# Optimization experiments

Measured on AMD Instinct MI355X. Metric: run time of the kernel, lower is better.

Reference implementation:

```python
import jax, jax.numpy as jnp
import numpy as np

THRESH = 0.1
BN_EPS = 1e-5
B, N, C_IN, C_HID, C_OUT = 4096, 128, 64, 256, 128


def setup_inputs() -> dict:
    key = jax.random.key(0)
    ks = jax.random.split(key, 10)
    a = jax.random.uniform(ks[0], (B, N, N), dtype=jnp.float32)
    v = jax.random.normal(ks[1], (B, N, C_IN), dtype=jnp.float32)
    # MLP params: Linear(C_IN->C_HID) + BN + ReLU + Linear(C_HID->C_OUT) + BN + ReLU
    W1 = jax.random.normal(ks[2], (C_IN, C_HID), dtype=jnp.float32) / np.sqrt(C_IN)
    b1 = jnp.zeros((C_HID,), jnp.float32)
    g1 = 1.0 + 0.1 * jax.random.normal(ks[3], (C_HID,), dtype=jnp.float32)
    be1 = 0.1 * jax.random.normal(ks[4], (C_HID,), dtype=jnp.float32)
    rm1 = 0.1 * jax.random.normal(ks[5], (C_HID,), dtype=jnp.float32)
    rv1 = jnp.ones((C_HID,), jnp.float32)
    W2 = jax.random.normal(ks[6], (C_HID, C_OUT), dtype=jnp.float32) / np.sqrt(C_HID)
    b2 = jnp.zeros((C_OUT,), jnp.float32)
    g2 = 1.0 + 0.1 * jax.random.normal(ks[7], (C_OUT,), dtype=jnp.float32)
    be2 = 0.1 * jax.random.normal(ks[8], (C_OUT,), dtype=jnp.float32)
    rm2 = 0.1 * jax.random.normal(ks[9], (C_OUT,), dtype=jnp.float32)
    rv2 = jnp.ones((C_OUT,), jnp.float32)
    return {"a": a, "v": v, "W1": W1, "b1": b1, "g1": g1, "be1": be1, "rm1": rm1, "rv1": rv1,
            "W2": W2, "b2": b2, "g2": g2, "be2": be2, "rm2": rm2, "rv2": rv2}


def reference(a, v, W1, b1, g1, be1, rm1, rv1, W2, b2, g2, be2, rm2, rv2):
    # threshold adjacency
    a_th = (a >= THRESH).astype(v.dtype)            # [B, N, N]
    # D^-0.5 A D^-0.5 as row/col rescaling (equivalent to diag_embed + bmm)
    d_inv_sqrt = jnp.sum(a_th, axis=-1) ** -0.5     # [B, N]
    a_bar = d_inv_sqrt[:, :, None] * a_th * d_inv_sqrt[:, None, :]
    # propagate
    h = jnp.einsum('bnm,bmc->bnc', a_bar, v)        # [B, N, C_IN]
    x = h.reshape(-1, h.shape[-1])                  # [(B N), C_IN]
    # MLP with BatchNorm in eval mode (running stats), dropout is identity in eval
    x = x @ W1 + b1
    x = (x - rm1) * jax.lax.rsqrt(rv1 + BN_EPS) * g1 + be1
    x = jax.nn.relu(x)
    x = x @ W2 + b2
    x = (x - rm2) * jax.lax.rsqrt(rv2 + BN_EPS) * g2 + be2
    x = jax.nn.relu(x)
    return x
```

## Files before the change

### kernel.cpp

```cpp
#include <hip/hip_runtime.h>


#define THRESH 0.1f
#define BN_EPS 1e-5f

typedef __attribute__((ext_vector_type(8))) short bf16x8;
typedef __attribute__((ext_vector_type(4))) float f32x4;

__device__ __forceinline__ unsigned short f2bf(float f) {
    union { float f; unsigned u; } x; x.f = f;
    unsigned r = x.u + 0x7FFFu + ((x.u >> 16) & 1u);
    return (unsigned short)(r >> 16);
}

__device__ __forceinline__ unsigned cvt_pk(float lo, float hi) {
    unsigned r;
    asm("v_cvt_pk_bf16_f32 %0, %1, %2" : "=v"(r) : "v"(lo), "v"(hi));
    return r;
}

__global__ void gcn_prep(const float* __restrict__ W1, const float* __restrict__ b1,
                         const float* __restrict__ g1, const float* __restrict__ be1,
                         const float* __restrict__ rm1, const float* __restrict__ rv1,
                         const float* __restrict__ W2, const float* __restrict__ b2,
                         const float* __restrict__ g2, const float* __restrict__ be2,
                         const float* __restrict__ rm2, const float* __restrict__ rv2,
                         unsigned short* __restrict__ W1s, unsigned short* __restrict__ W2s,
                         float* __restrict__ sh1, float* __restrict__ sh2) {
    int t = blockIdx.x * blockDim.x + threadIdx.x;
    if (t < 256 * 64) {
        int n = t >> 6, kp = t & 63;
        int sp = kp >> 3, lo = kp & 7;
        int s  = sp ^ (n & 7);
        int k2 = s * 8 + lo;
        int r = k2 & 3, aa = (k2 >> 2) & 1, gg = (k2 >> 3) & 3, T = k2 >> 5;
        int k = T * 32 + aa * 16 + gg * 4 + r;
        float sc = g1[n] * rsqrtf(rv1[n] + BN_EPS);
        W1s[t] = f2bf(W1[k * 256 + n] * sc);
    }
    {
        int n = t >> 8, kp = t & 255;
        int sp = kp >> 3, lo = kp & 7;
        int s  = sp ^ (n & 7);
        int k2 = s * 8 + lo;
        int r = k2 & 3, aa = (k2 >> 2) & 1, gg = (k2 >> 3) & 3, T = k2 >> 5;
        int k = T * 32 + aa * 16 + gg * 4 + r;
        float sc = g2[n] * rsqrtf(rv2[n] + BN_EPS);
        W2s[t] = f2bf(W2[k * 128 + n] * sc);
    }
    if (t < 256) {
        float s = g1[t] * rsqrtf(rv1[t] + BN_EPS);
        sh1[t] = (b1[t] - rm1[t]) * s + be1[t];
    }
    if (t < 128) {
        float s = g2[t] * rsqrtf(rv2[t] + BN_EPS);
        sh2[t] = (b2[t] - rm2[t]) * s + be2[t];
    }
}

__global__ void __launch_bounds__(256, 5)
gcn_prop(const float* __restrict__ A, const float* __restrict__ V,
         unsigned short* __restrict__ hP) {
    __shared__ unsigned short s_vtt[64 * 136];

    const int t    = threadIdx.x;
    const int lane = t & 63;
    const int w    = t >> 6;
    const int r16  = lane & 15;
    const int g    = lane >> 4;
    const int b    = blockIdx.x;

    const int mloc  = lane & 31;
    const int chalf = (lane >> 5) * 32;
    const float* vb = V + (size_t)b * 8192 + (size_t)(32 * w + mloc) * 64 + chalf;
    f32x4 pv[8];
#pragma unroll
    for (int q = 0; q < 8; ++q) pv[q] = *(const f32x4*)(vb + 4 * q);

    const float* ab = A + (size_t)b * 16384 + (size_t)(32 * w + r16) * 128;
    bf16x8 afrag[2][4];
    int cnt0 = 0, cnt1 = 0;
#pragma unroll
    for (int mt = 0; mt < 2; ++mt)
#pragma unroll
        for (int ks = 0; ks < 4; ++ks) {
            const float* p = ab + mt * 2048 + ks * 32 + 8 * g;
            f32x4 x0 = *(const f32x4*)p;
            f32x4 x1 = *(const f32x4*)(p + 4);
            union { unsigned short s[8]; bf16x8 v; } u;
            u.s[0] = (x0.x >= THRESH) ? (unsigned short)0x3F80u : (unsigned short)0u;
            u.s[1] = (x0.y >= THRESH) ? (unsigned short)0x3F80u : (unsigned short)0u;
            u.s[2] = (x0.z >= THRESH) ? (unsigned short)0x3F80u : (unsigned short)0u;
            u.s[3] = (x0.w >= THRESH) ? (unsigned short)0x3F80u : (unsigned short)0u;
            u.s[4] = (x1.x >= THRESH) ? (unsigned short)0x3F80u : (unsigned short)0u;
            u.s[5] = (x1.y >= THRESH) ? (unsigned short)0x3F80u : (unsigned short)0u;
            u.s[6] = (x1.z >= THRESH) ? (unsigned short)0x3F80u : (unsigned short)0u;
            u.s[7] = (x1.w >= THRESH) ? (unsigned short)0x3F80u : (unsigned short)0u;
            afrag[mt][ks] = u.v;
            int c = (x0.x >= THRESH) + (x0.y >= THRESH) + (x0.z >= THRESH) + (x0.w >= THRESH)
                  + (x1.x >= THRESH) + (x1.y >= THRESH) + (x1.z >= THRESH) + (x1.w >= THRESH);
            if (mt == 0) cnt0 += c; else cnt1 += c;
        }
    cnt0 += __shfl_xor(cnt0, 16); cnt0 += __shfl_xor(cnt0, 32);
    cnt1 += __shfl_xor(cnt1, 16); cnt1 += __shfl_xor(cnt1, 32);
    const float dinv0 = rsqrtf((float)cnt0);
    const float dinv1 = rsqrtf((float)cnt1);

    {
        float dm = (lane & 16) ? dinv1 : dinv0;
        int m = 32 * w + mloc;
#pragma unroll
        for (int q = 0; q < 8; ++q) {
            int c = chalf + 4 * q;
            s_vtt[(c + 0) * 136 + m] = f2bf(pv[q].x * dm);
            s_vtt[(c + 1) * 136 + m] = f2bf(pv[q].y * dm);
            s_vtt[(c + 2) * 136 + m] = f2bf(pv[q].z * dm);
            s_vtt[(c + 3) * 136 + m] = f2bf(pv[q].w * dm);
        }
    }
    __syncthreads();

    f32x4 acc1[4][2];
#pragma unroll
    for (int ct = 0; ct < 4; ++ct)
#pragma unroll
        for (int mt = 0; mt < 2; ++mt) acc1[ct][mt] = f32x4{0.f, 0.f, 0.f, 0.f};
#pragma unroll
    for (int ks = 0; ks < 4; ++ks)
#pragma unroll
        for (int ct = 0; ct < 4; ++ct) {
            bf16x8 av = *(const bf16x8*)(s_vtt + (ct * 16 + r16) * 136 + ks * 32 + 8 * g);
            acc1[ct][0] = __builtin_amdgcn_mfma_f32_16x16x32_bf16(av, afrag[0][ks], acc1[ct][0], 0, 0, 0);
            acc1[ct][1] = __builtin_amdgcn_mfma_f32_16x16x32_bf16(av, afrag[1][ks], acc1[ct][1], 0, 0, 0);
        }

#pragma unroll
    for (int mt = 0; mt < 2; ++mt) {
        float d = (mt == 0) ? dinv0 : dinv1;
        size_t m = (size_t)(b * 128 + 32 * w + 16 * mt + r16);
#pragma unroll
        for (int ks2 = 0; ks2 < 2; ++ks2) {
            union { unsigned u[4]; bf16x8 v; } pk;
            pk.u[0] = cvt_pk(acc1[2 * ks2][mt][0] * d,     acc1[2 * ks2][mt][1] * d);
            pk.u[1] = cvt_pk(acc1[2 * ks2][mt][2] * d,     acc1[2 * ks2][mt][3] * d);
            pk.u[2] = cvt_pk(acc1[2 * ks2 + 1][mt][0] * d, acc1[2 * ks2 + 1][mt][1] * d);
            pk.u[3] = cvt_pk(acc1[2 * ks2 + 1][mt][2] * d, acc1[2 * ks2 + 1][mt][3] * d);
            *(bf16x8*)(hP + m * 64 + ks2 * 32 + 8 * g) = pk.v;
        }
    }
}

__global__ void __launch_bounds__(512, 2)
gcn_mlp(const unsigned short* __restrict__ hP,
        const unsigned short* __restrict__ W1s, const unsigned short* __restrict__ W2s,
        const float* __restrict__ sh1g, const float* __restrict__ sh2g,
        float* __restrict__ out) {
    __shared__ char smem[99840];
    unsigned short* W1L = (unsigned short*)smem;
    unsigned short* W2L = (unsigned short*)(smem + 32768);
    float* s_sh1 = (float*)(smem + 98304);
    float* s_sh2 = (float*)(smem + 99328);

    const int t    = threadIdx.x;
    const int lane = t & 63;
    const int w    = t >> 6;
    const int r16  = lane & 15;
    const int g    = lane >> 4;

#pragma unroll
    for (int q = 0; q < 4; ++q)
        *(f32x4*)(smem + t * 64 + q * 16) = *(const f32x4*)((const char*)W1s + t * 64 + q * 16);
#pragma unroll
    for (int q = 0; q < 8; ++q)
        *(f32x4*)(smem + 32768 + t * 128 + q * 16) =
            *(const f32x4*)((const char*)W2s + t * 128 + q * 16);
    if (t < 256) s_sh1[t] = sh1g[t];
    if (t < 128) s_sh2[t] = sh2g[t];
    __syncthreads();

    const size_t row00 = (size_t)blockIdx.x * 1024;

    bf16x8 nb[2][2];
    {
        size_t mb = row00 + 32 * w;
#pragma unroll
        for (int mt = 0; mt < 2; ++mt)
#pragma unroll
            for (int ks2 = 0; ks2 < 2; ++ks2)
                nb[mt][ks2] = *(const bf16x8*)(hP + (mb + 16 * mt + r16) * 64 + ks2 * 32 + 8 * g);
    }

#pragma unroll 1
    for (int i = 0; i < 4; ++i) {
        bf16x8 bh[2][2];
#pragma unroll
        for (int mt = 0; mt < 2; ++mt)
#pragma unroll
            for (int ks2 = 0; ks2 < 2; ++ks2) bh[mt][ks2] = nb[mt][ks2];

        if (i < 3) {
            size_t mb = row00 + (i + 1) * 256 + 32 * w;
#pragma unroll
            for (int mt = 0; mt < 2; ++mt)
#pragma unroll
                for (int ks2 = 0; ks2 < 2; ++ks2)
                    nb[mt][ks2] = *(const bf16x8*)(hP + (mb + 16 * mt + r16) * 64 + ks2 * 32 + 8 * g);
        }

        f32x4 acc3[2][8];
#pragma unroll
        for (int mt = 0; mt < 2; ++mt)
#pragma unroll
            for (int ct = 0; ct < 8; ++ct) acc3[mt][ct] = f32x4{0.f, 0.f, 0.f, 0.f};

#pragma unroll
        for (int T = 0; T < 8; ++T) {
            f32x4 a2[2][2];
#pragma unroll
            for (int mt = 0; mt < 2; ++mt)
#pragma unroll
                for (int ctp = 0; ctp < 2; ++ctp) a2[mt][ctp] = f32x4{0.f, 0.f, 0.f, 0.f};
#pragma unroll
            for (int ctp = 0; ctp < 2; ++ctp) {
                int n = (2 * T + ctp) * 16 + r16;
#pragma unroll
                for (int ks2 = 0; ks2 < 2; ++ks2) {
                    int sp = (ks2 * 4 + g) ^ (n & 7);
                    bf16x8 aw = *(const bf16x8*)(W1L + n * 64 + sp * 8);
                    a2[0][ctp] = __builtin_amdgcn_mfma_f32_16x16x32_bf16(aw, bh[0][ks2], a2[0][ctp], 0, 0, 0);
                    a2[1][ctp] = __builtin_amdgcn_mfma_f32_16x16x32_bf16(aw, bh[1][ks2], a2[1][ctp], 0, 0, 0);
                }
            }
            unsigned wds[2][4];
#pragma unroll
            for (int ctp = 0; ctp < 2; ++ctp) {
                f32x4 sh = *(const f32x4*)(s_sh1 + (2 * T + ctp) * 16 + 4 * g);
#pragma unroll
                for (int mt = 0; mt < 2; ++mt) {
                    float y0 = fmaxf(a2[mt][ctp][0] + sh.x, 0.f);
                    float y1 = fmaxf(a2[mt][ctp][1] + sh.y, 0.f);
                    float y2 = fmaxf(a2[mt][ctp][2] + sh.z, 0.f);
                    float y3 = fmaxf(a2[mt][ctp][3] + sh.w, 0.f);
                    wds[mt][2 * ctp + 0] = cvt_pk(y0, y1);
                    wds[mt][2 * ctp + 1] = cvt_pk(y2, y3);
                }
            }
#pragma unroll
            for (int ct3 = 0; ct3 < 8; ++ct3) {
                int n  = ct3 * 16 + r16;
                int sp = (T * 4 + g) ^ (n & 7);
                bf16x8 bw = *(const bf16x8*)(W2L + n * 256 + sp * 8);
#pragma unroll
                for (int mt = 0; mt < 2; ++mt) {
                    union { unsigned u[4]; bf16x8 v; } af;
                    af.u[0] = wds[mt][0]; af.u[1] = wds[mt][1];
                    af.u[2] = wds[mt][2]; af.u[3] = wds[mt][3];
                    acc3[mt][ct3] = __builtin_amdgcn_mfma_f32_16x16x32_bf16(af.v, bw, acc3[mt][ct3], 0, 0, 0);
                }
            }
        }

        float* ob = out + (row00 + i * 256 + 32 * w) * 128;
#pragma unroll
        for (int ct3 = 0; ct3 < 8; ++ct3) {
            int c = ct3 * 16 + r16;
            float sh = s_sh2[c];
#pragma unroll
            for (int mt = 0; mt < 2; ++mt)
#pragma unroll
                for (int r = 0; r < 4; ++r) {
                    int row = 16 * mt + 4 * g + r;
                    ob[row * 128 + c] = fmaxf(acc3[mt][ct3][r] + sh, 0.f);
                }
        }
    }
}

extern "C" void kernel_launch(void* const* d_in, const int* in_sizes, int n_in,
                              void* d_out, int out_size, void* d_ws, size_t ws_size,
                              hipStream_t stream) {
    (void)in_sizes; (void)n_in; (void)out_size; (void)ws_size;
    const float* a   = (const float*)d_in[0];
    const float* v   = (const float*)d_in[1];
    const float* W1  = (const float*)d_in[2];
    const float* b1  = (const float*)d_in[3];
    const float* g1  = (const float*)d_in[4];
    const float* be1 = (const float*)d_in[5];
    const float* rm1 = (const float*)d_in[6];
    const float* rv1 = (const float*)d_in[7];
    const float* W2  = (const float*)d_in[8];
    const float* b2  = (const float*)d_in[9];
    const float* g2  = (const float*)d_in[10];
    const float* be2 = (const float*)d_in[11];
    const float* rm2 = (const float*)d_in[12];
    const float* rv2 = (const float*)d_in[13];

    char* ws = (char*)d_ws;
    unsigned short* W1s = (unsigned short*)ws;
    unsigned short* W2s = (unsigned short*)(ws + 32768);
    float* sh1 = (float*)(ws + 98304);
    float* sh2 = (float*)(ws + 99328);
    unsigned short* hP = (unsigned short*)(ws + 102400);

    gcn_prep<<<128, 256, 0, stream>>>(W1, b1, g1, be1, rm1, rv1,
                                      W2, b2, g2, be2, rm2, rv2,
                                      W1s, W2s, sh1, sh2);
    gcn_prop<<<4096, 256, 0, stream>>>(a, v, hP);
    gcn_mlp<<<512, 512, 0, stream>>>(hP, W1s, W2s, sh1, sh2, (float*)d_out);
}
```

Before: 227.0 us.

## Double per-wave row tile in MLP kernel and drop hP prefetch

Each wave in the MLP kernel now handles 64 rows (four 16-row M tiles) instead of 32, so every W1/W2 fragment read from LDS feeds twice as many MFMAs. The grid is halved to 256 blocks, each covering 2048 rows. The software prefetch of the next hP tile is removed and inputs are loaded at the start of each iteration. This trades higher register pressure (the acc3 accumulators double to 128 floats per lane), fewer blocks per CU for latency hiding, and exposed load latency for lower LDS traffic per MFMA.

Result: slower. 428.3 us (+88.7%).

```diff
diff --git a/kernel.cpp b/kernel.cpp
--- a/kernel.cpp
+++ b/kernel.cpp
@@ -178,46 +178,30 @@
     if (t < 128) s_sh2[t] = sh2g[t];
     __syncthreads();
 
-    const size_t row00 = (size_t)blockIdx.x * 1024;
-
-    bf16x8 nb[2][2];
-    {
-        size_t mb = row00 + 32 * w;
-#pragma unroll
-        for (int mt = 0; mt < 2; ++mt)
-#pragma unroll
-            for (int ks2 = 0; ks2 < 2; ++ks2)
-                nb[mt][ks2] = *(const bf16x8*)(hP + (mb + 16 * mt + r16) * 64 + ks2 * 32 + 8 * g);
-    }
+    const size_t row00 = (size_t)blockIdx.x * 2048;
 
 #pragma unroll 1
     for (int i = 0; i < 4; ++i) {
-        bf16x8 bh[2][2];
-#pragma unroll
-        for (int mt = 0; mt < 2; ++mt)
-#pragma unroll
-            for (int ks2 = 0; ks2 < 2; ++ks2) bh[mt][ks2] = nb[mt][ks2];
-
-        if (i < 3) {
-            size_t mb = row00 + (i + 1) * 256 + 32 * w;
-#pragma unroll
-            for (int mt = 0; mt < 2; ++mt)
-#pragma unroll
-                for (int ks2 = 0; ks2 < 2; ++ks2)
-                    nb[mt][ks2] = *(const bf16x8*)(hP + (mb + 16 * mt + r16) * 64 + ks2 * 32 + 8 * g);
-        }
-
-        f32x4 acc3[2][8];
-#pragma unroll
-        for (int mt = 0; mt < 2; ++mt)
+        const size_t mb = row00 + (size_t)i * 512 + 64 * w;
+
+        bf16x8 bh[4][2];
+#pragma unroll
+        for (int mt = 0; mt < 4; ++mt)
+#pragma unroll
+            for (int ks2 = 0; ks2 < 2; ++ks2)
+                bh[mt][ks2] = *(const bf16x8*)(hP + (mb + 16 * mt + r16) * 64 + ks2 * 32 + 8 * g);
+
+        f32x4 acc3[4][8];
+#pragma unroll
+        for (int mt = 0; mt < 4; ++mt)
 #pragma unroll
             for (int ct = 0; ct < 8; ++ct) acc3[mt][ct] = f32x4{0.f, 0.f, 0.f, 0.f};
 
 #pragma unroll
         for (int T = 0; T < 8; ++T) {
-            f32x4 a2[2][2];
-#pragma unroll
-            for (int mt = 0; mt < 2; ++mt)
+            f32x4 a2[4][2];
+#pragma unroll
+            for (int mt = 0; mt < 4; ++mt)
 #pragma unroll
                 for (int ctp = 0; ctp < 2; ++ctp) a2[mt][ctp] = f32x4{0.f, 0.f, 0.f, 0.f};
 #pragma unroll
@@ -227,22 +211,23 @@
                 for (int ks2 = 0; ks2 < 2; ++ks2) {
                     int sp = (ks2 * 4 + g) ^ (n & 7);
                     bf16x8 aw = *(const bf16x8*)(W1L + n * 64 + sp * 8);
-                    a2[0][ctp] = __builtin_amdgcn_mfma_f32_16x16x32_bf16(aw, bh[0][ks2], a2[0][ctp], 0, 0, 0);
-                    a2[1][ctp] = __builtin_amdgcn_mfma_f32_16x16x32_bf16(aw, bh[1][ks2], a2[1][ctp], 0, 0, 0);
+#pragma unroll
+                    for (int mt = 0; mt < 4; ++mt)
+                        a2[mt][ctp] = __builtin_amdgcn_mfma_f32_16x16x32_bf16(aw, bh[mt][ks2], a2[mt][ctp], 0, 0, 0);
                 }
             }
-            unsigned wds[2][4];
+            union { unsigned u[4]; bf16x8 v; } af[4];
 #pragma unroll
             for (int ctp = 0; ctp < 2; ++ctp) {
                 f32x4 sh = *(const f32x4*)(s_sh1 + (2 * T + ctp) * 16 + 4 * g);
 #pragma unroll
-                for (int mt = 0; mt < 2; ++mt) {
+                for (int mt = 0; mt < 4; ++mt) {
                     float y0 = fmaxf(a2[mt][ctp][0] + sh.x, 0.f);
                     float y1 = fmaxf(a2[mt][ctp][1] + sh.y, 0.f);
                     float y2 = fmaxf(a2[mt][ctp][2] + sh.z, 0.f);
                     float y3 = fmaxf(a2[mt][ctp][3] + sh.w, 0.f);
-                    wds[mt][2 * ctp + 0] = cvt_pk(y0, y1);
-                    wds[mt][2 * ctp + 1] = cvt_pk(y2, y3);
+                    af[mt].u[2 * ctp + 0] = cvt_pk(y0, y1);
+                    af[mt].u[2 * ctp + 1] = cvt_pk(y2, y3);
                 }
             }
 #pragma unroll
@@ -251,22 +236,18 @@
                 int sp = (T * 4 + g) ^ (n & 7);
                 bf16x8 bw = *(const bf16x8*)(W2L + n * 256 + sp * 8);
 #pragma unroll
-                for (int mt = 0; mt < 2; ++mt) {
-                    union { unsigned u[4]; bf16x8 v; } af;
-                    af.u[0] = wds[mt][0]; af.u[1] = wds[mt][1];
-                    af.u[2] = wds[mt][2]; af.u[3] = wds[mt][3];
-                    acc3[mt][ct3] = __builtin_amdgcn_mfma_f32_16x16x32_bf16(af.v, bw, acc3[mt][ct3], 0, 0, 0);
-                }
+                for (int mt = 0; mt < 4; ++mt)
+                    acc3[mt][ct3] = __builtin_amdgcn_mfma_f32_16x16x32_bf16(af[mt].v, bw, acc3[mt][ct3], 0, 0, 0);
             }
         }
 
-        float* ob = out + (row00 + i * 256 + 32 * w) * 128;
+        float* ob = out + mb * 128;
 #pragma unroll
         for (int ct3 = 0; ct3 < 8; ++ct3) {
             int c = ct3 * 16 + r16;
             float sh = s_sh2[c];
 #pragma unroll
-            for (int mt = 0; mt < 2; ++mt)
+            for (int mt = 0; mt < 4; ++mt)
 #pragma unroll
                 for (int r = 0; r < 4; ++r) {
                     int row = 16 * mt + 4 * g + r;
@@ -306,5 +287,5 @@
                                       W2, b2, g2, be2, rm2, rv2,
                                       W1s, W2s, sh1, sh2);
     gcn_prop<<<4096, 256, 0, stream>>>(a, v, hP);
-    gcn_mlp<<<512, 512, 0, stream>>>(hP, W1s, W2s, sh1, sh2, (float*)d_out);
-}
+    gcn_mlp<<<256, 512, 0, stream>>>(hP, W1s, W2s, sh1, sh2, (float*)d_out);
+}
```
